# Optimization experiments

Measured on AMD Instinct MI355X. Metric: run time of the kernel, lower is better.

The kernel has to match this reference:

```python
import jax, jax.numpy as jnp
import numpy as np

N_NODES = 50000
N_EDGES = 600000
IN_CH, HID_CH, OUT_CH = 128, 128, 64


def setup_inputs() -> dict:
    key = jax.random.key(0)
    ks = jax.random.split(key, 8)
    s = lambda fan_in: 1.0 / np.sqrt(fan_in)
    return {
        "x": jax.random.normal(ks[0], (N_NODES, IN_CH), dtype=jnp.float32),
        "edge_index": jax.random.randint(ks[1], (2, N_EDGES), 0, N_NODES, dtype=jnp.int32),
        "W1l": jax.random.normal(ks[2], (IN_CH, HID_CH), dtype=jnp.float32) * s(IN_CH),
        "W1r": jax.random.normal(ks[3], (IN_CH, HID_CH), dtype=jnp.float32) * s(IN_CH),
        "b1": jnp.zeros((HID_CH,), dtype=jnp.float32),
        "W2l": jax.random.normal(ks[4], (HID_CH, OUT_CH), dtype=jnp.float32) * s(HID_CH),
        "W2r": jax.random.normal(ks[5], (HID_CH, OUT_CH), dtype=jnp.float32) * s(HID_CH),
        "b2": jnp.zeros((OUT_CH,), dtype=jnp.float32),
    }


def _sage_conv(x, edge_index, Wl, Wr, b):
    """PyG SAGEConv (aggr='mean', root_weight=True): lin_l(mean_j x_j) + lin_r(x_i)."""
    src, dst = edge_index[0], edge_index[1]
    n = x.shape[0]
    # gather source features per edge, scatter-add into destination nodes
    agg = jax.ops.segment_sum(x[src], dst, num_segments=n)  # [N, F]
    deg = jax.ops.segment_sum(jnp.ones(src.shape, x.dtype), dst, num_segments=n)
    mean = agg / jnp.maximum(deg, 1.0)[:, None]
    return mean @ Wl + x @ Wr + b


def reference(x, edge_index, W1l, W1r, b1, W2l, W2r, b2):
    h = jax.nn.relu(_sage_conv(x, edge_index, W1l, W1r, b1))
    # dropout p=0.05 is identity in eval mode
    return _sage_conv(h, edge_index, W2l, W2r, b2)
```

## Files before the change

### kernel.cpp

```cpp
#include <hip/hip_runtime.h>
#include <hip/hip_bf16.h>

#define IN_CH 128
#define HID_CH 128
#define OUT_CH 64
#define SCAN_B 256

typedef __attribute__((ext_vector_type(8))) short bf16x8;
typedef __attribute__((ext_vector_type(4))) float f32x4;

__device__ __forceinline__ ushort f2bf(float f) {
    uint u = __float_as_uint(f);
    uint r = (u + 0x7fffu + ((u >> 16) & 1u)) >> 16;
    return (ushort)r;
}


__global__ void count_deg_kernel(const int* __restrict__ ei, int* __restrict__ deg,
                                 int n_edges) {
    int e = blockIdx.x * blockDim.x + threadIdx.x;
    if (e < n_edges) {
        atomicAdd(&deg[ei[n_edges + e]], 1);
    }
}

__global__ __launch_bounds__(SCAN_B) void scan_partials_kernel(
    const int* __restrict__ deg, int* __restrict__ partials, int n) {
    __shared__ int ws[SCAN_B / 64];
    int i = blockIdx.x * SCAN_B + threadIdx.x;
    int v = (i < n) ? deg[i] : 0;
    for (int off = 32; off > 0; off >>= 1) v += __shfl_down(v, off, 64);
    int lane = threadIdx.x & 63, w = threadIdx.x >> 6;
    if (lane == 0) ws[w] = v;
    __syncthreads();
    if (threadIdx.x == 0) {
        int s = 0;
        for (int k = 0; k < SCAN_B / 64; ++k) s += ws[k];
        partials[blockIdx.x] = s;
    }
}

__global__ __launch_bounds__(1024) void scan_bases_kernel(
    const int* __restrict__ partials, int* __restrict__ bases,
    int* __restrict__ offsets, int nblocks, int n) {
    __shared__ int sm[1024];
    int t = threadIdx.x;
    int v = (t < nblocks) ? partials[t] : 0;
    sm[t] = v;
    __syncthreads();
    for (int off = 1; off < 1024; off <<= 1) {
        int u = (t >= off) ? sm[t - off] : 0;
        __syncthreads();
        sm[t] += u;
        __syncthreads();
    }
    if (t < nblocks) bases[t] = sm[t] - v;
    if (t == 1023) offsets[n] = sm[1023];
}

__global__ __launch_bounds__(SCAN_B) void scan_final_kernel(
    const int* __restrict__ deg, const int* __restrict__ bases,
    int* __restrict__ offsets, int* __restrict__ cursor, int n) {
    __shared__ int sm[SCAN_B];
    int t = threadIdx.x;
    int i = blockIdx.x * SCAN_B + t;
    int v = (i < n) ? deg[i] : 0;
    sm[t] = v;
    __syncthreads();
    for (int off = 1; off < SCAN_B; off <<= 1) {
        int u = (t >= off) ? sm[t - off] : 0;
        __syncthreads();
        sm[t] += u;
        __syncthreads();
    }
    if (i < n) {
        int o = bases[blockIdx.x] + sm[t] - v;
        offsets[i] = o;
        cursor[i]  = o;
    }
}

__global__ void fill_kernel(const int* __restrict__ ei, int* __restrict__ cursor,
                            int* __restrict__ edge_src, int n_edges) {
    int e = blockIdx.x * blockDim.x + threadIdx.x;
    if (e < n_edges) {
        int s = ei[e];
        int d = ei[n_edges + e];
        int pos = atomicAdd(&cursor[d], 1);
        edge_src[pos] = s;
    }
}


__global__ void cvt_f32_bf16_kernel(const float* __restrict__ in,
                                    ushort* __restrict__ out, int n) {
    int i = blockIdx.x * blockDim.x + threadIdx.x;
    if (i * 4 >= n) return;
    float4 v = *(const float4*)(in + i * 4);
    ushort4 o;
    o.x = f2bf(v.x); o.y = f2bf(v.y); o.z = f2bf(v.z); o.w = f2bf(v.w);
    *(ushort4*)(out + i * 4) = o;
}

__global__ void transpose_bf16_kernel(const float* __restrict__ in,
                                      ushort* __restrict__ out, int K, int N) {
    int idx = blockIdx.x * blockDim.x + threadIdx.x;
    if (idx >= K * N) return;
    int nn = idx / K, kk = idx % K;
    out[idx] = f2bf(in[kk * N + nn]);
}


__global__ __launch_bounds__(256) void gather_mean_bf16_kernel(
    const ushort* __restrict__ feat, const int* __restrict__ offsets,
    const int* __restrict__ edge_src, ushort* __restrict__ mean, int n_nodes) {
    int wid  = (blockIdx.x * blockDim.x + threadIdx.x) >> 6;
    int lane = threadIdx.x & 63;
    if (wid >= n_nodes) return;
    int beg = offsets[wid];
    int end = offsets[wid + 1];
    float sx = 0.f, sy = 0.f;
    int e = beg;
    for (; e + 3 < end; e += 4) {
        uint a = *(const uint*)(feat + (size_t)edge_src[e]     * 128 + 2 * lane);
        uint b = *(const uint*)(feat + (size_t)edge_src[e + 1] * 128 + 2 * lane);
        uint c = *(const uint*)(feat + (size_t)edge_src[e + 2] * 128 + 2 * lane);
        uint d = *(const uint*)(feat + (size_t)edge_src[e + 3] * 128 + 2 * lane);
        sx += __uint_as_float(a << 16) + __uint_as_float(b << 16) +
              __uint_as_float(c << 16) + __uint_as_float(d << 16);
        sy += __uint_as_float(a & 0xffff0000u) + __uint_as_float(b & 0xffff0000u) +
              __uint_as_float(c & 0xffff0000u) + __uint_as_float(d & 0xffff0000u);
    }
    for (; e < end; ++e) {
        uint a = *(const uint*)(feat + (size_t)edge_src[e] * 128 + 2 * lane);
        sx += __uint_as_float(a << 16);
        sy += __uint_as_float(a & 0xffff0000u);
    }
    float inv = 1.0f / fmaxf((float)(end - beg), 1.0f);
    uint o = (uint)f2bf(sx * inv) | ((uint)f2bf(sy * inv) << 16);
    *(uint*)(mean + (size_t)wid * 128 + 2 * lane) = o;
}


__global__ __launch_bounds__(256) void l1_mfma_kernel(
    const ushort* __restrict__ mean, const ushort* __restrict__ xb,
    const ushort* __restrict__ WlT, const ushort* __restrict__ WrT,
    const float* __restrict__ b, ushort* __restrict__ h, int n_nodes) {
    int wave = threadIdx.x >> 6, lane = threadIdx.x & 63;
    int m0 = (blockIdx.x * 4 + wave) * 32;
    int r  = lane & 15;
    int ko = (lane >> 4) * 8;

    int gc0 = min(m0 + r,      n_nodes - 1);
    int gc1 = min(m0 + 16 + r, n_nodes - 1);

    f32x4 acc[8][2] = {};
#pragma unroll
    for (int kk = 0; kk < 4; ++kk) {
        int kb = kk * 32 + ko;
        bf16x8 aM0 = *(const bf16x8*)(mean + (size_t)gc0 * 128 + kb);
        bf16x8 aM1 = *(const bf16x8*)(mean + (size_t)gc1 * 128 + kb);
        bf16x8 aX0 = *(const bf16x8*)(xb   + (size_t)gc0 * 128 + kb);
        bf16x8 aX1 = *(const bf16x8*)(xb   + (size_t)gc1 * 128 + kb);
#pragma unroll
        for (int j = 0; j < 8; ++j) {
            bf16x8 bL = *(const bf16x8*)(WlT + (size_t)(j * 16 + r) * 128 + kb);
            bf16x8 bR = *(const bf16x8*)(WrT + (size_t)(j * 16 + r) * 128 + kb);
            acc[j][0] = __builtin_amdgcn_mfma_f32_16x16x32_bf16(aM0, bL, acc[j][0], 0, 0, 0);
            acc[j][0] = __builtin_amdgcn_mfma_f32_16x16x32_bf16(aX0, bR, acc[j][0], 0, 0, 0);
            acc[j][1] = __builtin_amdgcn_mfma_f32_16x16x32_bf16(aM1, bL, acc[j][1], 0, 0, 0);
            acc[j][1] = __builtin_amdgcn_mfma_f32_16x16x32_bf16(aX1, bR, acc[j][1], 0, 0, 0);
        }
    }

#pragma unroll
    for (int j = 0; j < 8; ++j) {
        float bv = b[j * 16 + r];
#pragma unroll
        for (int s = 0; s < 2; ++s) {
            int rowbase = m0 + s * 16 + (lane >> 4) * 4;
#pragma unroll
            for (int q = 0; q < 4; ++q) {
                int g = rowbase + q;
                if (g < n_nodes)
                    h[(size_t)g * 128 + j * 16 + r] =
                        f2bf(fmaxf(acc[j][s][q] + bv, 0.f));
            }
        }
    }
}


__global__ __launch_bounds__(256) void l2_mfma_kernel(
    const ushort* __restrict__ mean, const ushort* __restrict__ hb,
    const ushort* __restrict__ WlT, const ushort* __restrict__ WrT,
    const float* __restrict__ b, float* __restrict__ out, int n_nodes) {
    int wave = threadIdx.x >> 6, lane = threadIdx.x & 63;
    int m0 = (blockIdx.x * 4 + wave) * 32;
    int r  = lane & 15;
    int ko = (lane >> 4) * 8;

    int gc0 = min(m0 + r,      n_nodes - 1);
    int gc1 = min(m0 + 16 + r, n_nodes - 1);

    f32x4 acc[4][2] = {};
#pragma unroll
    for (int kk = 0; kk < 4; ++kk) {
        int kb = kk * 32 + ko;
        bf16x8 aM0 = *(const bf16x8*)(mean + (size_t)gc0 * 128 + kb);
        bf16x8 aM1 = *(const bf16x8*)(mean + (size_t)gc1 * 128 + kb);
        bf16x8 aH0 = *(const bf16x8*)(hb   + (size_t)gc0 * 128 + kb);
        bf16x8 aH1 = *(const bf16x8*)(hb   + (size_t)gc1 * 128 + kb);
#pragma unroll
        for (int j = 0; j < 4; ++j) {
            bf16x8 bL = *(const bf16x8*)(WlT + (size_t)(j * 16 + r) * 128 + kb);
            bf16x8 bR = *(const bf16x8*)(WrT + (size_t)(j * 16 + r) * 128 + kb);
            acc[j][0] = __builtin_amdgcn_mfma_f32_16x16x32_bf16(aM0, bL, acc[j][0], 0, 0, 0);
            acc[j][0] = __builtin_amdgcn_mfma_f32_16x16x32_bf16(aH0, bR, acc[j][0], 0, 0, 0);
            acc[j][1] = __builtin_amdgcn_mfma_f32_16x16x32_bf16(aM1, bL, acc[j][1], 0, 0, 0);
            acc[j][1] = __builtin_amdgcn_mfma_f32_16x16x32_bf16(aH1, bR, acc[j][1], 0, 0, 0);
        }
    }

#pragma unroll
    for (int j = 0; j < 4; ++j) {
        float bv = b[j * 16 + r];
#pragma unroll
        for (int s = 0; s < 2; ++s) {
            int rowbase = m0 + s * 16 + (lane >> 4) * 4;
#pragma unroll
            for (int q = 0; q < 4; ++q) {
                int g = rowbase + q;
                if (g < n_nodes)
                    out[(size_t)g * 64 + j * 16 + r] = acc[j][s][q] + bv;
            }
        }
    }
}


extern "C" void kernel_launch(void* const* d_in, const int* in_sizes, int n_in,
                              void* d_out, int out_size, void* d_ws, size_t ws_size,
                              hipStream_t stream) {
    const float* x   = (const float*)d_in[0];
    const int*   ei  = (const int*)d_in[1];
    const float* W1l = (const float*)d_in[2];
    const float* W1r = (const float*)d_in[3];
    const float* b1  = (const float*)d_in[4];
    const float* W2l = (const float*)d_in[5];
    const float* W2r = (const float*)d_in[6];
    const float* b2  = (const float*)d_in[7];
    float* out = (float*)d_out;

    int n_nodes = in_sizes[0] / IN_CH;
    int n_edges = in_sizes[1] / 2;
    int nsb = (n_nodes + SCAN_B - 1) / SCAN_B;

    char* ws = (char*)d_ws;
    int* deg      = (int*)ws;
    int* offsets  = deg + n_nodes;
    int* cursor   = offsets + n_nodes + 1;
    int* partials = cursor + n_nodes;
    int* bases    = partials + nsb;
    int* edge_src = bases + nsb;
    size_t off = ((size_t)(3 * n_nodes + 1 + 2 * nsb + n_edges)) * sizeof(int);
    off = (off + 255) & ~(size_t)255;
    ushort* xb    = (ushort*)(ws + off);
    ushort* meanb = xb    + (size_t)n_nodes * 128;
    ushort* hb    = meanb + (size_t)n_nodes * 128;
    ushort* W1lT  = hb    + (size_t)n_nodes * 128;
    ushort* W1rT  = W1lT + 128 * 128;
    ushort* W2lT  = W1rT + 128 * 128;
    ushort* W2rT  = W2lT + 64 * 128;

    hipMemsetAsync(deg, 0, n_nodes * sizeof(int), stream);

    const int TB = 256;
    int eblocks = (n_edges + TB - 1) / TB;
    count_deg_kernel<<<eblocks, TB, 0, stream>>>(ei, deg, n_edges);
    scan_partials_kernel<<<nsb, SCAN_B, 0, stream>>>(deg, partials, n_nodes);
    scan_bases_kernel<<<1, 1024, 0, stream>>>(partials, bases, offsets, nsb, n_nodes);
    scan_final_kernel<<<nsb, SCAN_B, 0, stream>>>(deg, bases, offsets, cursor, n_nodes);
    fill_kernel<<<eblocks, TB, 0, stream>>>(ei, cursor, edge_src, n_edges);

    int nx = n_nodes * IN_CH;
    cvt_f32_bf16_kernel<<<(nx / 4 + TB - 1) / TB, TB, 0, stream>>>(x, xb, nx);
    transpose_bf16_kernel<<<(128 * 128 + TB - 1) / TB, TB, 0, stream>>>(W1l, W1lT, 128, 128);
    transpose_bf16_kernel<<<(128 * 128 + TB - 1) / TB, TB, 0, stream>>>(W1r, W1rT, 128, 128);
    transpose_bf16_kernel<<<(128 * 64 + TB - 1) / TB, TB, 0, stream>>>(W2l, W2lT, 128, 64);
    transpose_bf16_kernel<<<(128 * 64 + TB - 1) / TB, TB, 0, stream>>>(W2r, W2rT, 128, 64);

    int gblocks = (n_nodes * 64 + TB - 1) / TB;
    int mblocks = (n_nodes + 127) / 128;

    gather_mean_bf16_kernel<<<gblocks, TB, 0, stream>>>(xb, offsets, edge_src, meanb, n_nodes);
    l1_mfma_kernel<<<mblocks, 256, 0, stream>>>(meanb, xb, W1lT, W1rT, b1, hb, n_nodes);

    gather_mean_bf16_kernel<<<gblocks, TB, 0, stream>>>(hb, offsets, edge_src, meanb, n_nodes);
    l2_mfma_kernel<<<mblocks, 256, 0, stream>>>(meanb, hb, W2lT, W2rT, b2, out, n_nodes);
}
```

Before: 268.1 us.

## Fuse preprocessing kernels, vectorize edge passes, and widen gather loads per edge

```diff
diff --git a/kernel.cpp b/kernel.cpp
--- a/kernel.cpp
+++ b/kernel.cpp
@@ -14,15 +14,61 @@
     uint r = (u + 0x7fffu + ((u >> 16) & 1u)) >> 16;
     return (ushort)r;
 }
-
-
-__global__ void count_deg_kernel(const int* __restrict__ ei, int* __restrict__ deg,
-                                 int n_edges) {
-    int e = blockIdx.x * blockDim.x + threadIdx.x;
-    if (e < n_edges) {
-        atomicAdd(&deg[ei[n_edges + e]], 1);
-    }
-}
+__device__ __forceinline__ float bflo(uint u) { return __uint_as_float(u << 16); }
+__device__ __forceinline__ float bfhi(uint u) { return __uint_as_float(u & 0xffff0000u); }
+
+
+__global__ __launch_bounds__(256) void prep_count_kernel(
+    const int* __restrict__ ei, int* __restrict__ deg,
+    const float* __restrict__ x, ushort* __restrict__ xb,
+    const float* __restrict__ W1l, const float* __restrict__ W1r,
+    const float* __restrict__ W2l, const float* __restrict__ W2r,
+    ushort* __restrict__ W1lT, ushort* __restrict__ W1rT,
+    ushort* __restrict__ W2lT, ushort* __restrict__ W2rT,
+    int n_edges, int nx, int cnt_blocks, int cvt_blocks) {
+    int b = blockIdx.x, tid = threadIdx.x;
+    if (b < cnt_blocks) {
+        int e4 = b * 256 + tid;
+        if (e4 * 4 < n_edges) {
+            int4 d = *(const int4*)(ei + n_edges + e4 * 4);
+            atomicAdd(&deg[d.x], 1);
+            atomicAdd(&deg[d.y], 1);
+            atomicAdd(&deg[d.z], 1);
+            atomicAdd(&deg[d.w], 1);
+        }
+    } else if (b < cnt_blocks + cvt_blocks) {
+        int i = (b - cnt_blocks) * 256 + tid;
+        if (i * 8 < nx) {
+            float4 v0 = *(const float4*)(x + i * 8);
+            float4 v1 = *(const float4*)(x + i * 8 + 4);
+            uint4 o;
+            o.x = (uint)f2bf(v0.x) | ((uint)f2bf(v0.y) << 16);
+            o.y = (uint)f2bf(v0.z) | ((uint)f2bf(v0.w) << 16);
+            o.z = (uint)f2bf(v1.x) | ((uint)f2bf(v1.y) << 16);
+            o.w = (uint)f2bf(v1.z) | ((uint)f2bf(v1.w) << 16);
+            *(uint4*)(xb + i * 8) = o;
+        }
+    } else {
+        int t = (b - cnt_blocks - cvt_blocks) * 256 + tid;
+        if (t < 16384) {
+            int nn = t >> 7, kk = t & 127;
+            W1lT[t] = f2bf(W1l[kk * 128 + nn]);
+        } else if (t < 32768) {
+            int u = t - 16384;
+            int nn = u >> 7, kk = u & 127;
+            W1rT[u] = f2bf(W1r[kk * 128 + nn]);
+        } else if (t < 40960) {
+            int u = t - 32768;
+            int nn = u >> 7, kk = u & 127;
+            W2lT[u] = f2bf(W2l[kk * 64 + nn]);
+        } else if (t < 49152) {
+            int u = t - 40960;
+            int nn = u >> 7, kk = u & 127;
+            W2rT[u] = f2bf(W2r[kk * 64 + nn]);
+        }
+    }
+}
+
 
 __global__ __launch_bounds__(SCAN_B) void scan_partials_kernel(
     const int* __restrict__ deg, int* __restrict__ partials, int n) {
@@ -40,22 +86,22 @@
     }
 }
 
-__global__ __launch_bounds__(1024) void scan_bases_kernel(
+__global__ __launch_bounds__(256) void scan_bases_kernel(
     const int* __restrict__ partials, int* __restrict__ bases,
     int* __restrict__ offsets, int nblocks, int n) {
-    __shared__ int sm[1024];
+    __shared__ int sm[256];
     int t = threadIdx.x;
     int v = (t < nblocks) ? partials[t] : 0;
     sm[t] = v;
     __syncthreads();
-    for (int off = 1; off < 1024; off <<= 1) {
+    for (int off = 1; off < 256; off <<= 1) {
         int u = (t >= off) ? sm[t - off] : 0;
         __syncthreads();
         sm[t] += u;
         __syncthreads();
     }
     if (t < nblocks) bases[t] = sm[t] - v;
-    if (t == 1023) offsets[n] = sm[1023];
+    if (t == 255) offsets[n] = sm[255];
 }
 
 __global__ __launch_bounds__(SCAN_B) void scan_final_kernel(
@@ -80,34 +126,17 @@
     }
 }
 
-__global__ void fill_kernel(const int* __restrict__ ei, int* __restrict__ cursor,
-                            int* __restrict__ edge_src, int n_edges) {
-    int e = blockIdx.x * blockDim.x + threadIdx.x;
-    if (e < n_edges) {
-        int s = ei[e];
-        int d = ei[n_edges + e];
-        int pos = atomicAdd(&cursor[d], 1);
-        edge_src[pos] = s;
-    }
-}
-
-
-__global__ void cvt_f32_bf16_kernel(const float* __restrict__ in,
-                                    ushort* __restrict__ out, int n) {
-    int i = blockIdx.x * blockDim.x + threadIdx.x;
-    if (i * 4 >= n) return;
-    float4 v = *(const float4*)(in + i * 4);
-    ushort4 o;
-    o.x = f2bf(v.x); o.y = f2bf(v.y); o.z = f2bf(v.z); o.w = f2bf(v.w);
-    *(ushort4*)(out + i * 4) = o;
-}
-
-__global__ void transpose_bf16_kernel(const float* __restrict__ in,
-                                      ushort* __restrict__ out, int K, int N) {
-    int idx = blockIdx.x * blockDim.x + threadIdx.x;
-    if (idx >= K * N) return;
-    int nn = idx / K, kk = idx % K;
-    out[idx] = f2bf(in[kk * N + nn]);
+__global__ __launch_bounds__(256) void fill_kernel(
+    const int* __restrict__ ei, int* __restrict__ cursor,
+    int* __restrict__ edge_src, int n_edges) {
+    int e4 = blockIdx.x * 256 + threadIdx.x;
+    if (e4 * 4 >= n_edges) return;
+    int4 s = *(const int4*)(ei + e4 * 4);
+    int4 d = *(const int4*)(ei + n_edges + e4 * 4);
+    edge_src[atomicAdd(&cursor[d.x], 1)] = s.x;
+    edge_src[atomicAdd(&cursor[d.y], 1)] = s.y;
+    edge_src[atomicAdd(&cursor[d.z], 1)] = s.z;
+    edge_src[atomicAdd(&cursor[d.w], 1)] = s.w;
 }
 
 
@@ -119,26 +148,64 @@
     if (wid >= n_nodes) return;
     int beg = offsets[wid];
     int end = offsets[wid + 1];
-    float sx = 0.f, sy = 0.f;
+    int q = lane >> 4;
+    int c = lane & 15;
+    float s0 = 0, s1 = 0, s2 = 0, s3 = 0, s4 = 0, s5 = 0, s6 = 0, s7 = 0;
+
     int e = beg;
-    for (; e + 3 < end; e += 4) {
-        uint a = *(const uint*)(feat + (size_t)edge_src[e]     * 128 + 2 * lane);
-        uint b = *(const uint*)(feat + (size_t)edge_src[e + 1] * 128 + 2 * lane);
-        uint c = *(const uint*)(feat + (size_t)edge_src[e + 2] * 128 + 2 * lane);
-        uint d = *(const uint*)(feat + (size_t)edge_src[e + 3] * 128 + 2 * lane);
-        sx += __uint_as_float(a << 16) + __uint_as_float(b << 16) +
-              __uint_as_float(c << 16) + __uint_as_float(d << 16);
-        sy += __uint_as_float(a & 0xffff0000u) + __uint_as_float(b & 0xffff0000u) +
-              __uint_as_float(c & 0xffff0000u) + __uint_as_float(d & 0xffff0000u);
-    }
-    for (; e < end; ++e) {
-        uint a = *(const uint*)(feat + (size_t)edge_src[e] * 128 + 2 * lane);
-        sx += __uint_as_float(a << 16);
-        sy += __uint_as_float(a & 0xffff0000u);
-    }
-    float inv = 1.0f / fmaxf((float)(end - beg), 1.0f);
-    uint o = (uint)f2bf(sx * inv) | ((uint)f2bf(sy * inv) << 16);
-    *(uint*)(mean + (size_t)wid * 128 + 2 * lane) = o;
+    for (; e + 8 <= end; e += 8) {
+        int r0 = edge_src[e + q];
+        int r1 = edge_src[e + 4 + q];
+        uint4 A = *(const uint4*)(feat + (size_t)r0 * 128 + c * 8);
+        uint4 B = *(const uint4*)(feat + (size_t)r1 * 128 + c * 8);
+        s0 += bflo(A.x) + bflo(B.x);  s1 += bfhi(A.x) + bfhi(B.x);
+        s2 += bflo(A.y) + bflo(B.y);  s3 += bfhi(A.y) + bfhi(B.y);
+        s4 += bflo(A.z) + bflo(B.z);  s5 += bfhi(A.z) + bfhi(B.z);
+        s6 += bflo(A.w) + bflo(B.w);  s7 += bfhi(A.w) + bfhi(B.w);
+    }
+    int rem = end - e;
+    if (rem > 0) {
+        int i0 = min(e + q, end - 1);
+        int i1 = min(e + 4 + q, end - 1);
+        int r0 = edge_src[i0];
+        int r1 = edge_src[i1];
+        uint4 A = *(const uint4*)(feat + (size_t)r0 * 128 + c * 8);
+        uint4 B = *(const uint4*)(feat + (size_t)r1 * 128 + c * 8);
+        if (q < rem) {
+            s0 += bflo(A.x);  s1 += bfhi(A.x);
+            s2 += bflo(A.y);  s3 += bfhi(A.y);
+            s4 += bflo(A.z);  s5 += bfhi(A.z);
+            s6 += bflo(A.w);  s7 += bfhi(A.w);
+        }
+        if (4 + q < rem) {
+            s0 += bflo(B.x);  s1 += bfhi(B.x);
+            s2 += bflo(B.y);  s3 += bfhi(B.y);
+            s4 += bflo(B.z);  s5 += bfhi(B.z);
+            s6 += bflo(B.w);  s7 += bfhi(B.w);
+        }
+    }
+
+#pragma unroll
+    for (int m = 16; m < 64; m <<= 1) {
+        s0 += __shfl_xor(s0, m, 64);
+        s1 += __shfl_xor(s1, m, 64);
+        s2 += __shfl_xor(s2, m, 64);
+        s3 += __shfl_xor(s3, m, 64);
+        s4 += __shfl_xor(s4, m, 64);
+        s5 += __shfl_xor(s5, m, 64);
+        s6 += __shfl_xor(s6, m, 64);
+        s7 += __shfl_xor(s7, m, 64);
+    }
+
+    if (q == 0) {
+        float inv = 1.0f / fmaxf((float)(end - beg), 1.0f);
+        uint4 o;
+        o.x = (uint)f2bf(s0 * inv) | ((uint)f2bf(s1 * inv) << 16);
+        o.y = (uint)f2bf(s2 * inv) | ((uint)f2bf(s3 * inv) << 16);
+        o.z = (uint)f2bf(s4 * inv) | ((uint)f2bf(s5 * inv) << 16);
+        o.w = (uint)f2bf(s6 * inv) | ((uint)f2bf(s7 * inv) << 16);
+        *(uint4*)(mean + (size_t)wid * 128 + c * 8) = o;
+    }
 }
 
 
@@ -276,19 +343,18 @@
     hipMemsetAsync(deg, 0, n_nodes * sizeof(int), stream);
 
     const int TB = 256;
-    int eblocks = (n_edges + TB - 1) / TB;
-    count_deg_kernel<<<eblocks, TB, 0, stream>>>(ei, deg, n_edges);
+    int nx = n_nodes * IN_CH;
+    int cnt_blocks = (n_edges / 4 + TB - 1) / TB;
+    int cvt_blocks = (nx / 8 + TB - 1) / TB;
+    int tr_blocks  = (49152 + TB - 1) / TB;
+
+    prep_count_kernel<<<cnt_blocks + cvt_blocks + tr_blocks, TB, 0, stream>>>(
+        ei, deg, x, xb, W1l, W1r, W2l, W2r, W1lT, W1rT, W2lT, W2rT,
+        n_edges, nx, cnt_blocks, cvt_blocks);
     scan_partials_kernel<<<nsb, SCAN_B, 0, stream>>>(deg, partials, n_nodes);
-    scan_bases_kernel<<<1, 1024, 0, stream>>>(partials, bases, offsets, nsb, n_nodes);
+    scan_bases_kernel<<<1, 256, 0, stream>>>(partials, bases, offsets, nsb, n_nodes);
     scan_final_kernel<<<nsb, SCAN_B, 0, stream>>>(deg, bases, offsets, cursor, n_nodes);
-    fill_kernel<<<eblocks, TB, 0, stream>>>(ei, cursor, edge_src, n_edges);
-
-    int nx = n_nodes * IN_CH;
-    cvt_f32_bf16_kernel<<<(nx / 4 + TB - 1) / TB, TB, 0, stream>>>(x, xb, nx);
-    transpose_bf16_kernel<<<(128 * 128 + TB - 1) / TB, TB, 0, stream>>>(W1l, W1lT, 128, 128);
-    transpose_bf16_kernel<<<(128 * 128 + TB - 1) / TB, TB, 0, stream>>>(W1r, W1rT, 128, 128);
-    transpose_bf16_kernel<<<(128 * 64 + TB - 1) / TB, TB, 0, stream>>>(W2l, W2lT, 128, 64);
-    transpose_bf16_kernel<<<(128 * 64 + TB - 1) / TB, TB, 0, stream>>>(W2r, W2rT, 128, 64);
+    fill_kernel<<<cnt_blocks, TB, 0, stream>>>(ei, cursor, edge_src, n_edges);
 
     int gblocks = (n_nodes * 64 + TB - 1) / TB;
     int mblocks = (n_nodes + 127) / 128;
```

New measurement: 248.0 us. 7.5% less time.
